# Optimization experiments

Measured on AMD Instinct MI355X. Metric: run time of the kernel, lower is better.

The kernel has to match this reference:

```python
import jax, jax.numpy as jnp
import numpy as np

B, GRID, IN_CO, OUT_CO = 32, 4096, 64, 64
T_EMB, N_MODES = 256, 512
M_HALF = N_MODES // 2 + 1  # 257 retained rFFT modes


def setup_inputs() -> dict:
    key = jax.random.key(0)
    ks = jax.random.split(key, 6)
    w_std = jnp.sqrt(1.0 / (2.0 * IN_CO))
    return {
        "x": jax.random.normal(ks[0], (B, GRID, IN_CO), jnp.float32),
        "t_emb": jax.random.normal(ks[1], (B, T_EMB), jnp.float32),
        "weights_real": jax.random.normal(ks[2], (M_HALF, IN_CO, OUT_CO), jnp.float32) * w_std,
        "weights_imag": jax.random.normal(ks[3], (M_HALF, IN_CO, OUT_CO), jnp.float32) * w_std,
        "dense_real": jax.random.normal(ks[4], (T_EMB, M_HALF), jnp.float32) * jnp.sqrt(1.0 / T_EMB),
        "dense_imag": jax.random.normal(ks[5], (T_EMB, M_HALF), jnp.float32) * jnp.sqrt(1.0 / T_EMB),
    }


def reference(x, t_emb, weights_real, weights_imag, dense_real, dense_imag):
    b, in_grid_sz, _ = x.shape
    m = weights_real.shape[0]  # n_modes//2 + 1
    weights = weights_real + 1j * weights_imag  # (m, in_co, out_co)
    # rFFT over the grid axis
    x_ft = jnp.fft.rfft(x, axis=-2, norm="forward")  # (b, grid//2+1, in_co) complex
    # time modulation per mode: Dense(real) + i*Dense(imag)
    t_tr = (t_emb @ dense_real) + 1j * (t_emb @ dense_imag)  # (b, m)
    # original einsum with eye == elementwise per-mode scale then per-mode matmul
    x_out = jnp.einsum("bmi,mio->bmo", x_ft[:, :m, :], weights) * t_tr[:, :, None]
    out_ft = jnp.zeros((b, in_grid_sz // 2 + 1, weights.shape[-1]), jnp.complex64)
    out_ft = out_ft.at[:, :m, :].set(x_out)
    return jnp.fft.irfft(out_ft, axis=-2, n=in_grid_sz, norm="forward")
```

## Files before the change

### kernel.cpp

```cpp
#include <hip/hip_runtime.h>
#include <hip/hip_bf16.h>

typedef short short8 __attribute__((ext_vector_type(8)));
typedef float f32x4 __attribute__((ext_vector_type(4)));
typedef const void __attribute__((address_space(1))) as1_void;
typedef void __attribute__((address_space(3))) as3_void;

__device__ __forceinline__ float sin_rev(float r) {
  float o; asm("v_sin_f32 %0, %1" : "=v"(o) : "v"(r)); return o;
}
__device__ __forceinline__ float cos_rev(float r) {
  float o; asm("v_cos_f32 %0, %1" : "=v"(o) : "v"(r)); return o;
}

#define INV4096 0.000244140625f
#define INV16   0.0625f

__global__ __launch_bounds__(256) void prep_kernel(__hip_bfloat16* __restrict__ F2,
                                                   __hip_bfloat16* __restrict__ Gm2,
                                                   const float* __restrict__ t_emb,
                                                   const float* __restrict__ dr,
                                                   const float* __restrict__ di,
                                                   float* __restrict__ Sr,
                                                   float* __restrict__ Si,
                                                   const float* __restrict__ x,
                                                   __hip_bfloat16* __restrict__ E,
                                                   __hip_bfloat16* __restrict__ O,
                                                   float* __restrict__ Xr256p,
                                                   float* __restrict__ x2048f,
                                                   const float* __restrict__ Wr,
                                                   const float* __restrict__ Wi,
                                                   __hip_bfloat16* __restrict__ Wb) {
  const int bid = blockIdx.x;
  const int tid = threadIdx.x;
  __shared__ float te[256];
  __shared__ float tileA[64][65];
  __shared__ float tileB[64][65];
  __shared__ float red[4][64];
  __shared__ float xm[64];

  if (bid < 512) {
    const int row = bid;
    const int m   = (row < 256) ? row : (row - 255);
    const bool is_cos = (row < 256);
    int n0 = tid * 8;
    union { short8 v; unsigned short u[8]; } pk;
#pragma unroll
    for (int j = 0; j < 8; ++j) {
      int ph = (m * (n0 + j)) & 4095;
      float v = is_cos ?  cos_rev((float)ph * INV4096)
                       : -sin_rev((float)ph * INV4096);
      __hip_bfloat16 h = __float2bfloat16(v);
      pk.u[j] = *(unsigned short*)&h;
    }
    *(short8*)&F2[(size_t)row * 2048 + n0] = pk.v;
  } else if (bid < 1024) {
    const int gb = bid - 512;
    int e  = tid * 8;
    int n  = gb * 4 + (e >> 9);
    int c0 = e & 511;
    union { short8 v; unsigned short u[8]; } pk;
#pragma unroll
    for (int j = 0; j < 8; ++j) {
      int cc = c0 + j;
      int k  = (cc < 256) ? cc : (cc - 255);
      int ph = (n * k) & 4095;
      float v = (cc < 256) ? cos_rev((float)ph * INV4096)
                           : sin_rev((float)ph * INV4096);
      __hip_bfloat16 h = __float2bfloat16(v);
      pk.u[j] = *(unsigned short*)&h;
    }
    *(short8*)&Gm2[(size_t)n * 512 + c0] = pk.v;
  } else if (bid < 1056) {
    int b = bid - 1024;
    te[tid] = t_emb[b * 256 + tid];
    __syncthreads();
    for (int m = tid; m < 257; m += 256) {
      float ar = 0.f, ai = 0.f;
      for (int t = 0; t < 256; ++t) {
        float e = te[t];
        ar += e * dr[t * 257 + m];
        ai += e * di[t * 257 + m];
      }
      float c = (m == 0 ? 1.0f : 2.0f) * (1.0f / 4096.0f);
      Sr[b * 257 + m] = ar * c;
      Si[b * 257 + m] = ai * c;
    }
  } else if (bid < 2080) {
    int idx = bid - 1056;
    int nt = idx & 31;
    int b  = idx >> 5;
    int n0 = nt * 64;
    int m0r = (63 - nt) * 64;
#pragma unroll
    for (int it = 0; it < 4; ++it) {
      int c = it * 256 + tid;
      int r = c >> 4, i4 = (c & 15) * 4;
      float4 v = *(const float4*)&x[((size_t)b * 4096 + n0 + r) * 64 + i4];
      tileA[r][i4 + 0] = v.x; tileA[r][i4 + 1] = v.y;
      tileA[r][i4 + 2] = v.z; tileA[r][i4 + 3] = v.w;
      float4 w = *(const float4*)&x[((size_t)b * 4096 + m0r + r) * 64 + i4];
      tileB[r][i4 + 0] = w.x; tileB[r][i4 + 1] = w.y;
      tileB[r][i4 + 2] = w.z; tileB[r][i4 + 3] = w.w;
    }
    if (tid < 64) xm[tid] = (nt > 0) ? x[((size_t)b * 4096 + (4096 - n0)) * 64 + tid] : 0.f;
    __syncthreads();
#pragma unroll
    for (int it = 0; it < 2; ++it) {
      int c  = it * 256 + tid;
      int i  = c >> 3;
      int ch = c & 7;
      union { short8 v; unsigned short u[8]; } pe, po;
#pragma unroll
      for (int jj = 0; jj < 8; ++jj) {
        int j = ch * 8 + jj;
        float a = tileA[j][i];
        float mir = (j == 0) ? xm[i] : tileB[64 - j][i];
        __hip_bfloat16 he = __float2bfloat16(a + mir);
        __hip_bfloat16 ho = __float2bfloat16(a - mir);
        pe.u[jj] = *(unsigned short*)&he;
        po.u[jj] = *(unsigned short*)&ho;
      }
      size_t base = ((size_t)b * 64 + i) * 2048 + n0 + ch * 8;
      *(short8*)&E[base] = pe.v;
      *(short8*)&O[base] = po.v;
    }
    {
      int i = tid & 63, g = tid >> 6;
      float acc = 0.f;
#pragma unroll
      for (int j = 0; j < 16; ++j) {
        float w = cos_rev((float)j * INV16);
        acc += w * (tileA[g * 16 + j][i] + tileB[g * 16 + j][i]);
      }
      red[g][i] = acc;
    }
    __syncthreads();
    if (tid < 64) {
      Xr256p[((size_t)b * 32 + nt) * 64 + tid] =
          red[0][tid] + red[1][tid] + red[2][tid] + red[3][tid];
      if (nt == 31) x2048f[b * 64 + tid] = tileB[0][tid];
    }
  } else {
    int idx  = bid - 2080;
    int k    = idx >> 2;
    int quad = idx & 3;
    const float* src = (quad < 2) ? (Wr + (size_t)k * 4096 + quad * 2048)
                                  : (Wi + (size_t)k * 4096 + (quad - 2) * 2048);
    __hip_bfloat16* dst = Wb + (size_t)k * 8192 + (quad < 2 ? quad * 2048 : 4096 + (quad - 2) * 2048);
    int e = tid * 8;
    float4 v0 = *(const float4*)&src[e];
    float4 v1 = *(const float4*)&src[e + 4];
    union { short8 v; unsigned short u[8]; } pk;
    float vv[8] = {v0.x, v0.y, v0.z, v0.w, v1.x, v1.y, v1.z, v1.w};
#pragma unroll
    for (int j = 0; j < 8; ++j) {
      __hip_bfloat16 h = __float2bfloat16(vv[j]);
      pk.u[j] = *(unsigned short*)&h;
    }
    *(short8*)&dst[e] = pk.v;
  }
}

template <int NF>
__device__ __forceinline__ void stage_tileT(const __hip_bfloat16* __restrict__ A, int lda, int m0,
                                            const __hip_bfloat16* __restrict__ B, int ldb, int n0,
                                            int kt, __hip_bfloat16* As, __hip_bfloat16* Bs,
                                            int tid) {
#pragma unroll
  for (int j = 0; j < 4; ++j) {
    int c   = j * 256 + tid;
    int row = c >> 3;
    int chg = (c & 7) ^ (row & 7);
    const __hip_bfloat16* ga = A + (size_t)(m0 + row) * lda + kt + chg * 8;
    __hip_bfloat16* la = As + (size_t)(j * 256 + (tid & 192)) * 8;
    __builtin_amdgcn_global_load_lds((as1_void*)ga, (as3_void*)la, 16, 0, 0);
  }
#pragma unroll
  for (int j = 0; j < NF; ++j) {
    int c   = j * 256 + tid;
    int row = c >> 3;
    int chg = (c & 7) ^ (row & 7);
    const __hip_bfloat16* gb = B + (size_t)(n0 + row) * ldb + kt + chg * 8;
    __hip_bfloat16* lb = Bs + (size_t)(j * 256 + (tid & 192)) * 8;
    __builtin_amdgcn_global_load_lds((as1_void*)gb, (as3_void*)lb, 16, 0, 0);
  }
}

template <int NF>
__device__ __forceinline__ void compute_stepT(const __hip_bfloat16* As, const __hip_bfloat16* Bs,
                                              int wr, int wc, int fr, int fq,
                                              f32x4 acc[4][NF]) {
#pragma unroll
  for (int kk = 0; kk < 2; ++kk) {
    short8 av[4], bv[NF];
#pragma unroll
    for (int m = 0; m < 4; ++m) {
      int row  = wr + m * 16 + fr;
      int slot = (fq + kk * 4) ^ (row & 7);
      av[m] = *(const short8*)(As + row * 64 + slot * 8);
    }
#pragma unroll
    for (int n = 0; n < NF; ++n) {
      int row  = wc + n * 16 + fr;
      int slot = (fq + kk * 4) ^ (row & 7);
      bv[n] = *(const short8*)(Bs + row * 64 + slot * 8);
    }
#pragma unroll
    for (int m = 0; m < 4; ++m)
#pragma unroll
      for (int n = 0; n < NF; ++n)
        acc[m][n] = __builtin_amdgcn_mfma_f32_16x16x32_bf16(av[m], bv[n], acc[m][n], 0, 0, 0);
  }
}

template <int NF>
__device__ __forceinline__ void gemm_coreT(const __hip_bfloat16* __restrict__ A, int lda, int m0,
                                           const __hip_bfloat16* __restrict__ B, int ldb, int n0,
                                           int k0, int ksteps,
                                           __hip_bfloat16* As, __hip_bfloat16* Bs,
                                           f32x4 acc[4][NF]) {
  const int tid  = threadIdx.x;
  const int lane = tid & 63;
  const int wv   = tid >> 6;
  const int wr   = (wv >> 1) * 64;
  const int wc   = (wv & 1) * (NF * 16);
  const int fr   = lane & 15;
  const int fq   = lane >> 4;

  for (int ks = 0; ks < ksteps; ++ks) {
    stage_tileT<NF>(A, lda, m0, B, ldb, n0, k0 + ks * 64, As, Bs, tid);
    __syncthreads();
    compute_stepT<NF>(As, Bs, wr, wc, fr, fq, acc);
    __syncthreads();
  }
}

__global__ __launch_bounds__(256) void gemm1_kernel(const __hip_bfloat16* __restrict__ F2,
                                                    const __hip_bfloat16* __restrict__ E,
                                                    const __hip_bfloat16* __restrict__ O,
                                                    __hip_bfloat16* __restrict__ C1,
                                                    int kchunk, int splitk) {
  __shared__ __hip_bfloat16 As[128 * 64];
  __shared__ __hip_bfloat16 Bs[128 * 64];
  int n0 = blockIdx.x * 128;
  int m0 = blockIdx.y * 128;
  int k0 = blockIdx.z * kchunk;
  const __hip_bfloat16* B = (m0 < 256) ? E : O;
  f32x4 acc[4][4];
#pragma unroll
  for (int m = 0; m < 4; ++m)
#pragma unroll
    for (int n = 0; n < 4; ++n)
#pragma unroll
      for (int r = 0; r < 4; ++r) acc[m][n][r] = 0.f;

  gemm_coreT<4>(F2, 2048, m0, B, 2048, n0, k0, kchunk >> 6, As, Bs, acc);

  const int lane = threadIdx.x & 63;
  const int wv   = threadIdx.x >> 6;
  const int wr   = (wv >> 1) * 64, wc = (wv & 1) * 64;
  const int fr   = lane & 15, fq = lane >> 4;
#pragma unroll
  for (int m = 0; m < 4; ++m)
#pragma unroll
    for (int n = 0; n < 4; ++n)
#pragma unroll
      for (int j = 0; j < 4; ++j) {
        int row = m0 + wr + m * 16 + fq * 4 + j;
        int col = n0 + wc + n * 16 + fr;
        C1[((size_t)row * splitk + blockIdx.z) * 2048 + col] = __float2bfloat16(acc[m][n][j]);
      }
}

__global__ __launch_bounds__(256) void mix_kernel(const __hip_bfloat16* __restrict__ C1,
                                                  const float* __restrict__ Xr256p,
                                                  const float* __restrict__ x2048f,
                                                  const __hip_bfloat16* __restrict__ Wb,
                                                  const float* __restrict__ Sr,
                                                  const float* __restrict__ Si,
                                                  __hip_bfloat16* __restrict__ Y2T,
                                                  __hip_bfloat16* __restrict__ Yx,
                                                  int splitk) {
  const int k = blockIdx.x;
  const int q = blockIdx.y;
  const int tid = threadIdx.x;
  __shared__ float wlr[4096];
  __shared__ float wli[4096];
  __shared__ float xs[2048];

  const __hip_bfloat16* wbg = Wb + (size_t)k * 8192;
  for (int c = tid; c < 1024; c += 256) {
    short8 v = *(const short8*)(wbg + c * 8);
    float* dst = (c < 512) ? &wlr[c * 8] : &wli[(c - 512) * 8];
#pragma unroll
    for (int j = 0; j < 8; ++j) {
      unsigned short u = (unsigned short)v[j];
      dst[j] = __bfloat162float(*(__hip_bfloat16*)&u);
    }
  }

  {
    const int part = tid >> 7;
    const int ln   = tid & 127;
    const int bi0  = q * 1024 + ln * 8;
    float f[8] = {0.f, 0.f, 0.f, 0.f, 0.f, 0.f, 0.f, 0.f};
    if (k < 256) {
      if (part == 0 || k > 0) {
        int row = part ? 255 + k : k;
        const __hip_bfloat16* src = C1 + (size_t)row * splitk * 2048 + bi0;
        for (int z = 0; z < splitk; ++z) {
          short8 v = *(const short8*)(src + (size_t)z * 2048);
#pragma unroll
          for (int j = 0; j < 8; ++j) {
            unsigned short u = (unsigned short)v[j];
            f[j] += __bfloat162float(*(__hip_bfloat16*)&u);
          }
        }
      }
      if (part == 0) {
        float par = (k & 1) ? -1.f : 1.f;
#pragma unroll
        for (int j = 0; j < 8; ++j) f[j] += par * x2048f[bi0 + j];
      }
    } else {
      if (part == 0) {
        const float* sp = Xr256p + (size_t)(bi0 >> 6) * 2048 + (bi0 & 63);
#pragma unroll 8
        for (int nt = 0; nt < 32; ++nt)
#pragma unroll
          for (int j = 0; j < 8; ++j) f[j] += sp[nt * 64 + j];
      } else {
        const __hip_bfloat16* src = C1 + (size_t)511 * splitk * 2048 + bi0;
        for (int z = 0; z < splitk; ++z) {
          short8 v = *(const short8*)(src + (size_t)z * 2048);
#pragma unroll
          for (int j = 0; j < 8; ++j) {
            unsigned short u = (unsigned short)v[j];
            f[j] += __bfloat162float(*(__hip_bfloat16*)&u);
          }
        }
      }
    }
#pragma unroll
    for (int j = 0; j < 8; ++j) xs[part * 1024 + ln * 8 + j] = f[j];
  }
  __syncthreads();

  const int o  = tid & 63;
  const int jj = tid >> 6;
  float pr[4] = {0.f, 0.f, 0.f, 0.f};
  float pi[4] = {0.f, 0.f, 0.f, 0.f};
#pragma unroll 4
  for (int i = 0; i < 64; ++i) {
    float wrv = wlr[i * 64 + o];
    float wiv = wli[i * 64 + o];
#pragma unroll
    for (int u = 0; u < 4; ++u) {
      int lb = (jj * 4 + u) * 64 + i;
      float xr = xs[lb], xi = xs[1024 + lb];
      pr[u] += xr * wrv - xi * wiv;
      pi[u] += xr * wiv + xi * wrv;
    }
  }
#pragma unroll
  for (int u = 0; u < 4; ++u) {
    int b = q * 16 + jj * 4 + u;
    float sr = Sr[b * 257 + k], si = Si[b * 257 + k];
    int bo = b * 64 + o;
    __hip_bfloat16 yr = __float2bfloat16(pr[u] * sr - pi[u] * si);
    __hip_bfloat16 yi = __float2bfloat16(pr[u] * si + pi[u] * sr);
    if (k < 256) Y2T[(size_t)bo * 512 + k] = yr;
    else         Yx[bo] = yr;
    if (k >= 1)  Y2T[(size_t)bo * 512 + 255 + k] = yi;
  }
}

__global__ __launch_bounds__(256) void gemm2_kernel(const __hip_bfloat16* __restrict__ Gm2,
                                                    const __hip_bfloat16* __restrict__ Y2T,
                                                    const __hip_bfloat16* __restrict__ Yx,
                                                    float* __restrict__ out) {
  __shared__ __hip_bfloat16 As[128 * 64];
  __shared__ __hip_bfloat16 Bs[64 * 64];
  __shared__ float red2[4][64];
  int n0 = blockIdx.x * 64;
  int m0 = blockIdx.y * 128;
  f32x4 accC[4][2], accS[4][2];
#pragma unroll
  for (int m = 0; m < 4; ++m)
#pragma unroll
    for (int n = 0; n < 2; ++n)
#pragma unroll
      for (int r = 0; r < 4; ++r) { accC[m][n][r] = 0.f; accS[m][n][r] = 0.f; }

  gemm_coreT<2>(Gm2, 512, m0, Y2T, 512, n0, 0,   4, As, Bs, accC);
  gemm_coreT<2>(Gm2, 512, m0, Y2T, 512, n0, 256, 4, As, Bs, accS);

  const int lane = threadIdx.x & 63;
  const int wv   = threadIdx.x >> 6;
  const int wr   = (wv >> 1) * 64, wc = (wv & 1) * 32;
  const int fr   = lane & 15, fq = lane >> 4;
  float yx[2];
#pragma unroll
  for (int n = 0; n < 2; ++n)
    yx[n] = __bfloat162float(Yx[n0 + wc + n * 16 + fr]);
#pragma unroll
  for (int m = 0; m < 4; ++m)
#pragma unroll
    for (int j = 0; j < 4; ++j) {
      int row = m0 + wr + m * 16 + fq * 4 + j;
      float g = cos_rev((float)(row & 15) * INV16);
#pragma unroll
      for (int n = 0; n < 2; ++n) {
        int col = n0 + wc + n * 16 + fr;
        int b = col >> 6, o = col & 63;
        float vC = accC[m][n][j] + g * yx[n];
        float vS = accS[m][n][j];
        out[((size_t)b * 4096 + row) * 64 + o] = vC - vS;
        if (row > 0)
          out[((size_t)b * 4096 + (4096 - row)) * 64 + o] = vC + vS;
      }
    }

  if (m0 == 0) {
    __syncthreads();
    const int tid = threadIdx.x;
    int col = tid & 63, grp = tid >> 6;
    int bo = n0 + col;
    float s = 0.f;
    for (int k = grp * 64; k < grp * 64 + 64; ++k) {
      float v = __bfloat162float(Y2T[(size_t)bo * 512 + k]);
      s += (k & 1) ? -v : v;
    }
    red2[grp][col] = s;
    __syncthreads();
    if (tid < 64) {
      int bo2 = n0 + tid;
      float alt = red2[0][tid] + red2[1][tid] + red2[2][tid] + red2[3][tid]
                + __bfloat162float(Yx[bo2]);
      int b = bo2 >> 6, o = bo2 & 63;
      out[((size_t)b * 4096 + 2048) * 64 + o] = alt;
    }
  }
}

extern "C" void kernel_launch(void* const* d_in, const int* in_sizes, int n_in,
                              void* d_out, int out_size, void* d_ws, size_t ws_size,
                              hipStream_t stream) {
  const float* x  = (const float*)d_in[0];
  const float* te = (const float*)d_in[1];
  const float* wr = (const float*)d_in[2];
  const float* wi = (const float*)d_in[3];
  const float* dr = (const float*)d_in[4];
  const float* di = (const float*)d_in[5];
  float* out = (float*)d_out;

  char* p = (char*)d_ws;
  auto alloc = [&](size_t bytes) -> char* {
    char* r = p;
    p += (bytes + 255) & ~(size_t)255;
    return r;
  };
  __hip_bfloat16* F2  = (__hip_bfloat16*)alloc(512ull * 2048 * 2);
  __hip_bfloat16* Gm2 = (__hip_bfloat16*)alloc(2048ull * 512 * 2);
  __hip_bfloat16* E   = (__hip_bfloat16*)alloc(2048ull * 2048 * 2);
  __hip_bfloat16* O   = (__hip_bfloat16*)alloc(2048ull * 2048 * 2);
  float* Xr256p = (float*)alloc(32ull * 32 * 64 * 4);
  float* x2048f = (float*)alloc(2048 * 4);
  float* Sr = (float*)alloc(32 * 257 * 4);
  float* Si = (float*)alloc(32 * 257 * 4);
  __hip_bfloat16* Y2T = (__hip_bfloat16*)alloc(2048ull * 512 * 2);
  __hip_bfloat16* Yx  = (__hip_bfloat16*)alloc(2048 * 2);
  __hip_bfloat16* Wb  = (__hip_bfloat16*)alloc(257ull * 8192 * 2);
  size_t fixed = (size_t)(p - (char*)d_ws);

  int splitk = 2;
  if (ws_size >= fixed + 8ull * 512 * 2048 * 2)      splitk = 8;
  else if (ws_size >= fixed + 4ull * 512 * 2048 * 2) splitk = 4;
  __hip_bfloat16* C1 = (__hip_bfloat16*)alloc((size_t)splitk * 512 * 2048 * 2);
  int kchunk = 2048 / splitk;

  prep_kernel<<<3108, 256, 0, stream>>>(F2, Gm2, te, dr, di, Sr, Si, x, E, O,
                                        Xr256p, x2048f, wr, wi, Wb);
  gemm1_kernel<<<dim3(16, 4, splitk), 256, 0, stream>>>(F2, E, O, C1, kchunk, splitk);
  mix_kernel<<<dim3(257, 2), 256, 0, stream>>>(C1, Xr256p, x2048f, Wb, Sr, Si, Y2T, Yx, splitk);
  gemm2_kernel<<<dim3(32, 16), 256, 0, stream>>>(Gm2, Y2T, Yx, out);
}
```

Measured before the change: 84.88 us.

## Load fp32 spectral weights directly in mix kernel and cap split-K at four

Removes the weight bf16 conversion blocks from the prep kernel and has the mix kernel read the fp32 real and imaginary weights straight into shared memory, dropping the Wb round trip. The mix kernel's C1 reduction branches are reorganised by part/k. Maximum split-K for the first GEMM drops from 8 to 4, lowering the partial-sum traffic the mix kernel must reduce but giving gemm1 fewer blocks. Mix now reads twice the weight bytes from global memory.

```diff
diff --git a/kernel.cpp b/kernel.cpp
--- a/kernel.cpp
+++ b/kernel.cpp
@@ -27,10 +27,7 @@
                                                    __hip_bfloat16* __restrict__ E,
                                                    __hip_bfloat16* __restrict__ O,
                                                    float* __restrict__ Xr256p,
-                                                   float* __restrict__ x2048f,
-                                                   const float* __restrict__ Wr,
-                                                   const float* __restrict__ Wi,
-                                                   __hip_bfloat16* __restrict__ Wb) {
+                                                   float* __restrict__ x2048f) {
   const int bid = blockIdx.x;
   const int tid = threadIdx.x;
   __shared__ float te[256];
@@ -86,7 +83,7 @@
       Sr[b * 257 + m] = ar * c;
       Si[b * 257 + m] = ai * c;
     }
-  } else if (bid < 2080) {
+  } else {
     int idx = bid - 1056;
     int nt = idx & 31;
     int b  = idx >> 5;
@@ -141,24 +138,6 @@
           red[0][tid] + red[1][tid] + red[2][tid] + red[3][tid];
       if (nt == 31) x2048f[b * 64 + tid] = tileB[0][tid];
     }
-  } else {
-    int idx  = bid - 2080;
-    int k    = idx >> 2;
-    int quad = idx & 3;
-    const float* src = (quad < 2) ? (Wr + (size_t)k * 4096 + quad * 2048)
-                                  : (Wi + (size_t)k * 4096 + (quad - 2) * 2048);
-    __hip_bfloat16* dst = Wb + (size_t)k * 8192 + (quad < 2 ? quad * 2048 : 4096 + (quad - 2) * 2048);
-    int e = tid * 8;
-    float4 v0 = *(const float4*)&src[e];
-    float4 v1 = *(const float4*)&src[e + 4];
-    union { short8 v; unsigned short u[8]; } pk;
-    float vv[8] = {v0.x, v0.y, v0.z, v0.w, v1.x, v1.y, v1.z, v1.w};
-#pragma unroll
-    for (int j = 0; j < 8; ++j) {
-      __hip_bfloat16 h = __float2bfloat16(vv[j]);
-      pk.u[j] = *(unsigned short*)&h;
-    }
-    *(short8*)&dst[e] = pk.v;
   }
 }
 
@@ -276,7 +255,8 @@
 __global__ __launch_bounds__(256) void mix_kernel(const __hip_bfloat16* __restrict__ C1,
                                                   const float* __restrict__ Xr256p,
                                                   const float* __restrict__ x2048f,
-                                                  const __hip_bfloat16* __restrict__ Wb,
+                                                  const float* __restrict__ Wr,
+                                                  const float* __restrict__ Wi,
                                                   const float* __restrict__ Sr,
                                                   const float* __restrict__ Si,
                                                   __hip_bfloat16* __restrict__ Y2T,
@@ -289,15 +269,11 @@
   __shared__ float wli[4096];
   __shared__ float xs[2048];
 
-  const __hip_bfloat16* wbg = Wb + (size_t)k * 8192;
+  const float* wrg = Wr + (size_t)k * 4096;
+  const float* wig = Wi + (size_t)k * 4096;
   for (int c = tid; c < 1024; c += 256) {
-    short8 v = *(const short8*)(wbg + c * 8);
-    float* dst = (c < 512) ? &wlr[c * 8] : &wli[(c - 512) * 8];
-#pragma unroll
-    for (int j = 0; j < 8; ++j) {
-      unsigned short u = (unsigned short)v[j];
-      dst[j] = __bfloat162float(*(__hip_bfloat16*)&u);
-    }
+    *(float4*)&wlr[c * 4] = *(const float4*)&wrg[c * 4];
+    *(float4*)&wli[c * 4] = *(const float4*)&wig[c * 4];
   }
 
   {
@@ -305,10 +281,9 @@
     const int ln   = tid & 127;
     const int bi0  = q * 1024 + ln * 8;
     float f[8] = {0.f, 0.f, 0.f, 0.f, 0.f, 0.f, 0.f, 0.f};
-    if (k < 256) {
-      if (part == 0 || k > 0) {
-        int row = part ? 255 + k : k;
-        const __hip_bfloat16* src = C1 + (size_t)row * splitk * 2048 + bi0;
+    if (part == 0) {
+      if (k < 256) {
+        const __hip_bfloat16* src = C1 + (size_t)k * splitk * 2048 + bi0;
         for (int z = 0; z < splitk; ++z) {
           short8 v = *(const short8*)(src + (size_t)z * 2048);
 #pragma unroll
@@ -317,28 +292,24 @@
             f[j] += __bfloat162float(*(__hip_bfloat16*)&u);
           }
         }
-      }
-      if (part == 0) {
         float par = (k & 1) ? -1.f : 1.f;
 #pragma unroll
         for (int j = 0; j < 8; ++j) f[j] += par * x2048f[bi0 + j];
-      }
-    } else {
-      if (part == 0) {
+      } else {
         const float* sp = Xr256p + (size_t)(bi0 >> 6) * 2048 + (bi0 & 63);
 #pragma unroll 8
         for (int nt = 0; nt < 32; ++nt)
 #pragma unroll
           for (int j = 0; j < 8; ++j) f[j] += sp[nt * 64 + j];
-      } else {
-        const __hip_bfloat16* src = C1 + (size_t)511 * splitk * 2048 + bi0;
-        for (int z = 0; z < splitk; ++z) {
-          short8 v = *(const short8*)(src + (size_t)z * 2048);
-#pragma unroll
-          for (int j = 0; j < 8; ++j) {
-            unsigned short u = (unsigned short)v[j];
-            f[j] += __bfloat162float(*(__hip_bfloat16*)&u);
-          }
+      }
+    } else if (k > 0) {
+      const __hip_bfloat16* src = C1 + (size_t)(255 + k) * splitk * 2048 + bi0;
+      for (int z = 0; z < splitk; ++z) {
+        short8 v = *(const short8*)(src + (size_t)z * 2048);
+#pragma unroll
+        for (int j = 0; j < 8; ++j) {
+          unsigned short u = (unsigned short)v[j];
+          f[j] += __bfloat162float(*(__hip_bfloat16*)&u);
         }
       }
     }
@@ -471,18 +442,16 @@
   float* Si = (float*)alloc(32 * 257 * 4);
   __hip_bfloat16* Y2T = (__hip_bfloat16*)alloc(2048ull * 512 * 2);
   __hip_bfloat16* Yx  = (__hip_bfloat16*)alloc(2048 * 2);
-  __hip_bfloat16* Wb  = (__hip_bfloat16*)alloc(257ull * 8192 * 2);
   size_t fixed = (size_t)(p - (char*)d_ws);
 
   int splitk = 2;
-  if (ws_size >= fixed + 8ull * 512 * 2048 * 2)      splitk = 8;
-  else if (ws_size >= fixed + 4ull * 512 * 2048 * 2) splitk = 4;
+  if (ws_size >= fixed + 4ull * 512 * 2048 * 2) splitk = 4;
   __hip_bfloat16* C1 = (__hip_bfloat16*)alloc((size_t)splitk * 512 * 2048 * 2);
   int kchunk = 2048 / splitk;
 
-  prep_kernel<<<3108, 256, 0, stream>>>(F2, Gm2, te, dr, di, Sr, Si, x, E, O,
-                                        Xr256p, x2048f, wr, wi, Wb);
+  prep_kernel<<<2080, 256, 0, stream>>>(F2, Gm2, te, dr, di, Sr, Si, x, E, O,
+                                        Xr256p, x2048f);
   gemm1_kernel<<<dim3(16, 4, splitk), 256, 0, stream>>>(F2, E, O, C1, kchunk, splitk);
-  mix_kernel<<<dim3(257, 2), 256, 0, stream>>>(C1, Xr256p, x2048f, Wb, Sr, Si, Y2T, Yx, splitk);
+  mix_kernel<<<dim3(257, 2), 256, 0, stream>>>(C1, Xr256p, x2048f, wr, wi, Sr, Si, Y2T, Yx, splitk);
   gemm2_kernel<<<dim3(32, 16), 256, 0, stream>>>(Gm2, Y2T, Yx, out);
 }
```

Result: no change. 85.88 us (+1.2%).
